# Performance work log

Measured on AMD Instinct MI355X. Metric: run time of the kernel, lower is better.

Reference implementation:

```python
import jax, jax.numpy as jnp
import numpy as np

INPUT, HIDDEN = 2048, 64

def _gru_layer(x, W_ih, W_hh, b_ih, b_hh):
    # x: [B, T, D]; returns full output sequence [B, T, H]
    B, T, _ = x.shape
    H = W_hh.shape[1]
    # precompute input projections for all timesteps: [T, B, 3H]
    xi = jnp.einsum('btd,gd->tbg', x, W_ih) + b_ih
    h0 = jnp.zeros((B, H), dtype=x.dtype)

    def step(h, xt):
        hp = h @ W_hh.T + b_hh                      # [B, 3H]
        r = jax.nn.sigmoid(xt[:, :H] + hp[:, :H])
        z = jax.nn.sigmoid(xt[:, H:2*H] + hp[:, H:2*H])
        n = jnp.tanh(xt[:, 2*H:] + r * hp[:, 2*H:])
        h_new = (1.0 - z) * n + z * h
        return h_new, h_new

    _, ys = jax.lax.scan(step, h0, xi)              # ys: [T, B, H]
    return jnp.transpose(ys, (1, 0, 2))


def setup_inputs() -> dict:
    key = jax.random.key(0)
    ks = jax.random.split(key, 12)
    B, T = 64, 512
    s0 = 1.0 / np.sqrt(HIDDEN)  # PyTorch GRU init scale
    u = lambda k, shape: jax.random.uniform(k, shape, jnp.float32, -s0, s0)
    return {
        'x': jax.random.normal(ks[0], (B, T, INPUT), jnp.float32),
        'W_ih0': u(ks[1], (3 * HIDDEN, INPUT)),
        'W_hh0': u(ks[2], (3 * HIDDEN, HIDDEN)),
        'b_ih0': u(ks[3], (3 * HIDDEN,)),
        'b_hh0': u(ks[4], (3 * HIDDEN,)),
        'W_ih1': u(ks[5], (3 * HIDDEN, HIDDEN)),
        'W_hh1': u(ks[6], (3 * HIDDEN, HIDDEN)),
        'b_ih1': u(ks[7], (3 * HIDDEN,)),
        'b_hh1': u(ks[8], (3 * HIDDEN,)),
        'fc_w': u(ks[9], (1, HIDDEN)),
        'fc_b': u(ks[10], (1,)),
    }


def reference(x, W_ih0, W_hh0, b_ih0, b_hh0, W_ih1, W_hh1, b_ih1, b_hh1, fc_w, fc_b):
    y0 = _gru_layer(x, W_ih0, W_hh0, b_ih0, b_hh0)   # [B, T, H]
    y1 = _gru_layer(y0, W_ih1, W_hh1, b_ih1, b_hh1)  # [B, T, H]
    h_last = y1[:, -1, :]                            # h_n of top layer
    return h_last @ fc_w.T + fc_b                    # [B, 1]
```

## Files before the change

kernel.cpp:

```cpp
#include <hip/hip_runtime.h>

#define T_STEPS 512
#define BATCH   64
#define HID     64
#define G3      192
#define DIN     2048
#define B_BLK   16
#define NBLK    4
#define LOG2E   1.44269504088896340736f
#define LDP     196
#define NROUND  130

typedef float    f32x4    __attribute__((ext_vector_type(4)));
typedef short    short8   __attribute__((ext_vector_type(8)));
typedef unsigned uint32x4 __attribute__((ext_vector_type(4)));

__device__ __forceinline__ unsigned short f2bf(float f) {
    unsigned int u = __builtin_bit_cast(unsigned int, f);
    unsigned int r = u + 0x7fffu + ((u >> 16) & 1u);
    return (unsigned short)(r >> 16);
}
__device__ __forceinline__ unsigned int cvtpk(float a, float b) {
    unsigned int r;
    asm("v_cvt_pk_bf16_f32 %0, %1, %2" : "=v"(r) : "v"(a), "v"(b));
    return r;
}
__device__ __forceinline__ float exp2neg(float x) {
    float r; asm("v_exp_f32 %0, -%1" : "=v"(r) : "v"(x)); return r;
}
__device__ __forceinline__ float exp2pos(float x) {
    float r; asm("v_exp_f32 %0, %1" : "=v"(r) : "v"(x)); return r;
}
__device__ __forceinline__ void wg_barrier() {
    asm volatile("s_waitcnt lgkmcnt(0)" ::: "memory");
    __builtin_amdgcn_s_barrier();
    asm volatile("" ::: "memory");
}
__device__ __forceinline__ void sig_flag(volatile unsigned* f, unsigned v) {
    asm volatile("s_waitcnt lgkmcnt(0)" ::: "memory");
    *f = v;
}
__device__ __forceinline__ void wait_flags(const unsigned* base, unsigned tag) {
    const unsigned addr = (unsigned)(unsigned long long)base;
    for (;;) {
        uint32x4 f;
        asm volatile("ds_read_b128 %0, %1\n\ts_waitcnt lgkmcnt(0)"
                     : "=v"(f) : "v"(addr) : "memory");
        unsigned m0 = f.x < f.y ? f.x : f.y;
        unsigned m1 = f.z < f.w ? f.z : f.w;
        if ((m0 < m1 ? m0 : m1) >= tag) break;
    }
    asm volatile("" ::: "memory");
}

__device__ __forceinline__ float gunit(float grs, float gzs, float a2,
                                       float xn, float h) {
    float R   = 1.f + exp2neg(grs);
    float Q   = 1.f + exp2neg(gzs);
    float r   = __builtin_amdgcn_rcpf(R);
    float s   = fmaf(r, a2, xn);
    float P   = 1.f + exp2pos(s);
    float ipq = __builtin_amdgcn_rcpf(P * Q);
    float n   = fmaf(-2.f, ipq * Q, 1.f);
    return fmaf(h - n, ipq * P, n);
}

#define BM  128
#define BK  64
#define LDA 72
#define LDB 72

__launch_bounds__(512, 1)
__global__ void proj0_kernel(const float* __restrict__ x,
                             const float* __restrict__ Wih0,
                             const float* __restrict__ bih0,
                             float* __restrict__ xi)
{
    __shared__ unsigned short Asm[BM * LDA];
    __shared__ unsigned short Bsm[G3 * LDB];

    const int tid  = threadIdx.x;
    const int wave = tid >> 6;
    const int lane = tid & 63;
    const int wm   = wave >> 2;
    const int wn   = wave & 3;
    const int m0   = blockIdx.x * BM;
    const int l16  = lane & 15;
    const int lk   = lane >> 4;
    const int rA   = tid >> 4;
    const int c4   = tid & 15;

    const float* xb = x    + (size_t)(m0 + rA) * DIN + c4 * 4;
    const float* wb = Wih0 + (size_t)rA        * DIN + c4 * 4;
    unsigned short* ap = Asm + rA * LDA + c4 * 4;
    unsigned short* bp = Bsm + rA * LDB + c4 * 4;

    f32x4 acc[4][3];
#pragma unroll
    for (int mi = 0; mi < 4; ++mi)
#pragma unroll
        for (int ni = 0; ni < 3; ++ni)
            acc[mi][ni] = (f32x4){0.f, 0.f, 0.f, 0.f};

    float4 stA[4], stB[6];
#pragma unroll
    for (int it = 0; it < 4; ++it) stA[it] = *(const float4*)(xb + it * 32 * DIN);
#pragma unroll
    for (int it = 0; it < 6; ++it) stB[it] = *(const float4*)(wb + it * 32 * DIN);

    for (int kt = 0; kt < DIN / BK; ++kt) {
#pragma unroll
        for (int it = 0; it < 4; ++it) {
            uint2 pk;
            pk.x = cvtpk(stA[it].x, stA[it].y);
            pk.y = cvtpk(stA[it].z, stA[it].w);
            *(uint2*)(ap + it * 32 * LDA) = pk;
        }
#pragma unroll
        for (int it = 0; it < 6; ++it) {
            uint2 pk;
            pk.x = cvtpk(stB[it].x, stB[it].y);
            pk.y = cvtpk(stB[it].z, stB[it].w);
            *(uint2*)(bp + it * 32 * LDB) = pk;
        }
        if (kt + 1 < DIN / BK) {
            const int kk = (kt + 1) * BK;
#pragma unroll
            for (int it = 0; it < 4; ++it) stA[it] = *(const float4*)(xb + kk + it * 32 * DIN);
#pragma unroll
            for (int it = 0; it < 6; ++it) stB[it] = *(const float4*)(wb + kk + it * 32 * DIN);
        }
        wg_barrier();

#pragma unroll
        for (int ks = 0; ks < 2; ++ks) {
            const int kb = ks * 32 + lk * 8;
            short8 a[4], bfr[3];
#pragma unroll
            for (int mi = 0; mi < 4; ++mi)
                a[mi] = *(const short8*)&Asm[(wm * 64 + mi * 16 + l16) * LDA + kb];
#pragma unroll
            for (int ni = 0; ni < 3; ++ni)
                bfr[ni] = *(const short8*)&Bsm[(wn * 48 + ni * 16 + l16) * LDB + kb];
#pragma unroll
            for (int mi = 0; mi < 4; ++mi)
#pragma unroll
                for (int ni = 0; ni < 3; ++ni)
                    acc[mi][ni] = __builtin_amdgcn_mfma_f32_16x16x32_bf16(
                        a[mi], bfr[ni], acc[mi][ni], 0, 0, 0);
        }
        wg_barrier();
    }

#pragma unroll
    for (int ni = 0; ni < 3; ++ni) {
        int g = wn * 48 + ni * 16 + l16;
        float sc = (g < 128) ? LOG2E : 2.f * LOG2E;
        float bias = bih0[g];
#pragma unroll
        for (int mi = 0; mi < 4; ++mi) {
#pragma unroll
            for (int r = 0; r < 4; ++r) {
                int m  = m0 + wm * 64 + mi * 16 + lk * 4 + r;
                int t  = m & 511;
                int bb = m >> 9;
                xi[(size_t)(t * BATCH + bb) * G3 + g] = (acc[mi][ni][r] + bias) * sc;
            }
        }
    }
}

__launch_bounds__(768, 1)
__global__ void gru_fused_kernel(const float* __restrict__ xi,
                                 const float* __restrict__ Whh0,
                                 const float* __restrict__ bhh0,
                                 const float* __restrict__ Wih1,
                                 const float* __restrict__ bih1,
                                 const float* __restrict__ Whh1,
                                 const float* __restrict__ bhh1,
                                 const float* __restrict__ fcw,
                                 const float* __restrict__ fcb,
                                 float* __restrict__ out)
{
    __shared__ __align__(16) unsigned short h0d[8][8][B_BLK][8];
    __shared__ __align__(16) unsigned short h1d[8][8][B_BLK][8];
    __shared__ __align__(16) float pbuf[8][B_BLK][LDP];
    __shared__ float fcbuf[B_BLK][68];
    __shared__ __align__(16) unsigned h0flag[4];
    __shared__ __align__(16) unsigned h1flag[4];

    const int tid  = threadIdx.x;
    const int w    = tid >> 6;
    const int l    = tid & 63;
    const int c    = l & 15;
    const int kg   = l >> 4;
    const int blk  = blockIdx.x;
    const int role = w >> 2;
    const int sub  = w & 3;
    const int jw   = sub * 16;

    short8 frag[6];
    f32x4  bC[3];
    {
        const float* Wsel = (role == 0) ? Whh0 : (role == 1) ? Wih1 : Whh1;
#pragma unroll
        for (int g = 0; g < 3; ++g) {
            const float sc = (g == 2) ? 2.f * LOG2E : LOG2E;
#pragma unroll
            for (int ks = 0; ks < 2; ++ks) {
                const size_t roff = (size_t)(g * 64 + jw + c) * HID + ks * 32 + kg * 8;
                short8 s;
#pragma unroll
                for (int j = 0; j < 8; ++j) s[j] = (short)f2bf(Wsel[roff + j] * sc);
                frag[g * 2 + ks] = s;
            }
            float4 vh0 = *(const float4*)&bhh0[g * 64 + jw + kg * 4];
            float4 vi1 = *(const float4*)&bih1[g * 64 + jw + kg * 4];
            float4 vh1 = *(const float4*)&bhh1[g * 64 + jw + kg * 4];
            if (role == 0) {
                bC[g] = (f32x4){vh0.x * sc, vh0.y * sc, vh0.z * sc, vh0.w * sc};
            } else if (role == 1) {
                if (g < 2)
                    bC[g] = (f32x4){(vi1.x + vh1.x) * sc, (vi1.y + vh1.y) * sc,
                                    (vi1.z + vh1.z) * sc, (vi1.w + vh1.w) * sc};
                else
                    bC[g] = (f32x4){vi1.x * sc, vi1.y * sc, vi1.z * sc, vi1.w * sc};
            } else {
                if (g < 2) bC[g] = (f32x4){0.f, 0.f, 0.f, 0.f};
                else       bC[g] = (f32x4){vh1.x * sc, vh1.y * sc, vh1.z * sc, vh1.w * sc};
            }
        }
    }

    float hst[4] = {0.f, 0.f, 0.f, 0.f};

    for (int i = tid; i < 4096; i += 768) {
        ((unsigned int*)h0d)[i] = 0;
        ((unsigned int*)h1d)[i] = 0;
    }
    if (tid < 4) { h0flag[tid] = 0; h1flag[tid] = 0; }
    __syncthreads();

    const int chunk = 2 * sub + (kg >> 1);
    const int coff  = (kg & 1) * 4;

    if (role == 0) {
        __builtin_amdgcn_s_setprio(2);
        const size_t xstep = (size_t)BATCH * G3;
        const float* xp = xi + (size_t)(blk * B_BLK + c) * G3 + jw + kg * 4;
        float4 pA[3], pB[3];
        pA[0] = *(const float4*)(xp);
        pA[1] = *(const float4*)(xp + 64);
        pA[2] = *(const float4*)(xp + 128);
        pB[0] = *(const float4*)(xp + xstep);
        pB[1] = *(const float4*)(xp + xstep + 64);
        pB[2] = *(const float4*)(xp + xstep + 128);
        const float* xpr = xp + 2 * xstep;

        auto stepL0 = [&](int t, int s, float4 (&cur)[3]) {
            if (s > 0) {
                __builtin_amdgcn_s_setprio(0);
                wait_flags(h0flag, (unsigned)t);
                __builtin_amdgcn_s_setprio(2);
            }
            const int pb = (t + 7) & 7;
            short8 x0 = *(const short8*)&h0d[pb][kg][c][0];
            short8 x1 = *(const short8*)&h0d[pb][4 + kg][c][0];
            f32x4 a0 = bC[0], a1 = bC[1], a2 = bC[2];
            a0 = __builtin_amdgcn_mfma_f32_16x16x32_bf16(frag[0], x0, a0, 0, 0, 0);
            a0 = __builtin_amdgcn_mfma_f32_16x16x32_bf16(frag[1], x1, a0, 0, 0, 0);
            a1 = __builtin_amdgcn_mfma_f32_16x16x32_bf16(frag[2], x0, a1, 0, 0, 0);
            a1 = __builtin_amdgcn_mfma_f32_16x16x32_bf16(frag[3], x1, a1, 0, 0, 0);
            a2 = __builtin_amdgcn_mfma_f32_16x16x32_bf16(frag[4], x0, a2, 0, 0, 0);
            a2 = __builtin_amdgcn_mfma_f32_16x16x32_bf16(frag[5], x1, a2, 0, 0, 0);

            float4 xr4 = cur[0], xz4 = cur[1], xn4 = cur[2];
            if (t + 2 < T_STEPS) {
                cur[0] = *(const float4*)(xpr);
                cur[1] = *(const float4*)(xpr + 64);
                cur[2] = *(const float4*)(xpr + 128);
                xpr += xstep;
            }
            hst[0] = gunit(xr4.x + a0[0], xz4.x + a1[0], a2[0], xn4.x, hst[0]);
            hst[1] = gunit(xr4.y + a0[1], xz4.y + a1[1], a2[1], xn4.y, hst[1]);
            hst[2] = gunit(xr4.z + a0[2], xz4.z + a1[2], a2[2], xn4.z, hst[2]);
            hst[3] = gunit(xr4.w + a0[3], xz4.w + a1[3], a2[3], xn4.w, hst[3]);
            uint2 hw;
            hw.x = cvtpk(hst[0], hst[1]);
            hw.y = cvtpk(hst[2], hst[3]);
            *(uint2*)&h0d[t & 7][chunk][c][coff] = hw;
            if (s < 3) sig_flag(&h0flag[sub], (unsigned)(t + 1));
        };

        for (int r = 0; r < NROUND; ++r) {
            if (r < 128) {
                const int t0 = 4 * r;
                stepL0(t0 + 0, 0, pA);
                stepL0(t0 + 1, 1, pB);
                stepL0(t0 + 2, 2, pA);
                stepL0(t0 + 3, 3, pB);
            }
            wg_barrier();
        }
    } else if (role == 1) {
        auto stepP = [&](int k) {
            const int pb = k & 7;
            short8 x0 = *(const short8*)&h0d[pb][kg][c][0];
            short8 x1 = *(const short8*)&h0d[pb][4 + kg][c][0];
            f32x4 p0 = bC[0], p1 = bC[1], p2 = bC[2];
            p0 = __builtin_amdgcn_mfma_f32_16x16x32_bf16(frag[0], x0, p0, 0, 0, 0);
            p0 = __builtin_amdgcn_mfma_f32_16x16x32_bf16(frag[1], x1, p0, 0, 0, 0);
            p1 = __builtin_amdgcn_mfma_f32_16x16x32_bf16(frag[2], x0, p1, 0, 0, 0);
            p1 = __builtin_amdgcn_mfma_f32_16x16x32_bf16(frag[3], x1, p1, 0, 0, 0);
            p2 = __builtin_amdgcn_mfma_f32_16x16x32_bf16(frag[4], x0, p2, 0, 0, 0);
            p2 = __builtin_amdgcn_mfma_f32_16x16x32_bf16(frag[5], x1, p2, 0, 0, 0);
            float* pd = &pbuf[k & 7][c][jw + kg * 4];
            *(f32x4*)(pd)       = p0;
            *(f32x4*)(pd + 64)  = p1;
            *(f32x4*)(pd + 128) = p2;
        };
        for (int r = 0; r < NROUND; ++r) {
            if (r >= 1 && r <= 128) {
                const int k0 = 4 * r - 4;
                stepP(k0 + 0);
                stepP(k0 + 1);
                stepP(k0 + 2);
                stepP(k0 + 3);
            }
            wg_barrier();
        }
    } else {
        auto stepL1 = [&](int k, int s) {
            if (s > 0) wait_flags(h1flag, (unsigned)k);
            const int py = (k + 7) & 7;
            short8 y0 = *(const short8*)&h1d[py][kg][c][0];
            short8 y1 = *(const short8*)&h1d[py][4 + kg][c][0];
            f32x4 g0 = bC[0], g1 = bC[1], g2 = bC[2];
            g0 = __builtin_amdgcn_mfma_f32_16x16x32_bf16(frag[0], y0, g0, 0, 0, 0);
            g0 = __builtin_amdgcn_mfma_f32_16x16x32_bf16(frag[1], y1, g0, 0, 0, 0);
            g1 = __builtin_amdgcn_mfma_f32_16x16x32_bf16(frag[2], y0, g1, 0, 0, 0);
            g1 = __builtin_amdgcn_mfma_f32_16x16x32_bf16(frag[3], y1, g1, 0, 0, 0);
            g2 = __builtin_amdgcn_mfma_f32_16x16x32_bf16(frag[4], y0, g2, 0, 0, 0);
            g2 = __builtin_amdgcn_mfma_f32_16x16x32_bf16(frag[5], y1, g2, 0, 0, 0);

            const float* pd = &pbuf[k & 7][c][jw + kg * 4];
            f32x4 pr = *(const f32x4*)(pd);
            f32x4 pz = *(const f32x4*)(pd + 64);
            f32x4 pn = *(const f32x4*)(pd + 128);
#pragma unroll
            for (int q = 0; q < 4; ++q)
                hst[q] = gunit(pr[q] + g0[q], pz[q] + g1[q], g2[q], pn[q], hst[q]);
            uint2 hw;
            hw.x = cvtpk(hst[0], hst[1]);
            hw.y = cvtpk(hst[2], hst[3]);
            *(uint2*)&h1d[k & 7][chunk][c][coff] = hw;
            if (s < 3) sig_flag(&h1flag[sub], (unsigned)(k + 1));
        };
        for (int r = 0; r < NROUND; ++r) {
            if (r >= 2) {
                const int k0 = 4 * r - 8;
                stepL1(k0 + 0, 0);
                stepL1(k0 + 1, 1);
                stepL1(k0 + 2, 2);
                stepL1(k0 + 3, 3);
            }
            wg_barrier();
        }
    }

    if (role == 2) {
#pragma unroll
        for (int q = 0; q < 4; ++q)
            fcbuf[c][jw + kg * 4 + q] = hst[q];
    }
    __syncthreads();
    if (w == 0) {
        float p = 0.f;
#pragma unroll
        for (int jj = 0; jj < 16; ++jj)
            p += fcbuf[c][kg * 16 + jj] * fcw[kg * 16 + jj];
        p += __shfl_xor(p, 16);
        p += __shfl_xor(p, 32);
        if (kg == 0) out[blk * B_BLK + c] = p + fcb[0];
    }
}

extern "C" void kernel_launch(void* const* d_in, const int* in_sizes, int n_in,
                              void* d_out, int out_size, void* d_ws, size_t ws_size,
                              hipStream_t stream)
{
    const float* x    = (const float*)d_in[0];
    const float* Wih0 = (const float*)d_in[1];
    const float* Whh0 = (const float*)d_in[2];
    const float* bih0 = (const float*)d_in[3];
    const float* bhh0 = (const float*)d_in[4];
    const float* Wih1 = (const float*)d_in[5];
    const float* Whh1 = (const float*)d_in[6];
    const float* bih1 = (const float*)d_in[7];
    const float* bhh1 = (const float*)d_in[8];
    const float* fcw  = (const float*)d_in[9];
    const float* fcb  = (const float*)d_in[10];
    float* out = (float*)d_out;
    float* xi  = (float*)d_ws;

    hipLaunchKernelGGL(proj0_kernel, dim3(32768 / BM), dim3(512), 0, stream,
                       x, Wih0, bih0, xi);
    hipLaunchKernelGGL(gru_fused_kernel, dim3(NBLK), dim3(768), 0, stream,
                       xi, Whh0, bhh0, Wih1, bih1, Whh1, bhh1, fcw, fcb, out);
}
```

Measured before the change: 344.8 us.

## Fuse input projection into recurrent kernel with per-chunk ready flags

Merges the layer-0 input projection GEMM and the recurrent GRU kernel into one launch. Blocks 0-3 run the recurrence and blocks 4+ compute projection tiles ordered by time chunk, publishing completion through global atomic counters. The recurrence spins on those counters so it can start before the whole projection finishes. The projection output is also stored as bf16 to halve its traffic. This adds spin-wait and forward-progress risk (it relies on the recurrent blocks being co-resident with the producer blocks) and lowers the precision of the intermediate.

```diff
diff --git a/kernel.cpp b/kernel.cpp
--- a/kernel.cpp
+++ b/kernel.cpp
@@ -6,10 +6,13 @@
 #define G3      192
 #define DIN     2048
 #define B_BLK   16
-#define NBLK    4
 #define LOG2E   1.44269504088896340736f
 #define LDP     196
 #define NROUND  130
+#define LDA     72
+#define LDB     72
+#define PBM     64
+#define PBK     64
 
 typedef float    f32x4    __attribute__((ext_vector_type(4)));
 typedef short    short8   __attribute__((ext_vector_type(8)));
@@ -24,6 +27,12 @@
     unsigned int r;
     asm("v_cvt_pk_bf16_f32 %0, %1, %2" : "=v"(r) : "v"(a), "v"(b));
     return r;
+}
+__device__ __forceinline__ float bflo(unsigned int u) {
+    return __builtin_bit_cast(float, u << 16);
+}
+__device__ __forceinline__ float bfhi(unsigned int u) {
+    return __builtin_bit_cast(float, u & 0xffff0000u);
 }
 __device__ __forceinline__ float exp2neg(float x) {
     float r; asm("v_exp_f32 %0, -%1" : "=v"(r) : "v"(x)); return r;
@@ -51,6 +60,10 @@
         if ((m0 < m1 ? m0 : m1) >= tag) break;
     }
     asm volatile("" ::: "memory");
+}
+__device__ __forceinline__ void wait_chunk(const unsigned* cp) {
+    while (__hip_atomic_load(cp, __ATOMIC_ACQUIRE, __HIP_MEMORY_SCOPE_AGENT) < 16u)
+        __builtin_amdgcn_s_sleep(8);
 }
 
 __device__ __forceinline__ float gunit(float grs, float gzs, float a2,
@@ -65,131 +78,135 @@
     return fmaf(h - n, ipq * P, n);
 }
 
-#define BM  128
-#define BK  64
-#define LDA 72
-#define LDB 72
-
-__launch_bounds__(512, 1)
-__global__ void proj0_kernel(const float* __restrict__ x,
+struct GruS {
+    unsigned h0flag[4];
+    unsigned h1flag[4];
+    unsigned short h0d[8][8][B_BLK][8];
+    unsigned short h1d[8][8][B_BLK][8];
+    float pbuf[8][B_BLK][LDP];
+    float fcbuf[B_BLK][68];
+};
+struct ProjS {
+    unsigned short Asm[PBM * LDA];
+    unsigned short Bsm[G3 * LDB];
+};
+#define SMEM_BYTES 137504
+
+__global__ void zero_flags_kernel(unsigned* cnt) {
+    if (threadIdx.x < 64) cnt[threadIdx.x] = 0;
+}
+
+__launch_bounds__(768, 1)
+__global__ void fused_kernel(const float* __restrict__ x,
                              const float* __restrict__ Wih0,
                              const float* __restrict__ bih0,
-                             float* __restrict__ xi)
+                             const float* __restrict__ Whh0,
+                             const float* __restrict__ bhh0,
+                             const float* __restrict__ Wih1,
+                             const float* __restrict__ bih1,
+                             const float* __restrict__ Whh1,
+                             const float* __restrict__ bhh1,
+                             const float* __restrict__ fcw,
+                             const float* __restrict__ fcb,
+                             unsigned short* __restrict__ xi,
+                             unsigned* __restrict__ cnt,
+                             float* __restrict__ out)
 {
-    __shared__ unsigned short Asm[BM * LDA];
-    __shared__ unsigned short Bsm[G3 * LDB];
-
-    const int tid  = threadIdx.x;
-    const int wave = tid >> 6;
-    const int lane = tid & 63;
-    const int wm   = wave >> 2;
-    const int wn   = wave & 3;
-    const int m0   = blockIdx.x * BM;
-    const int l16  = lane & 15;
-    const int lk   = lane >> 4;
-    const int rA   = tid >> 4;
-    const int c4   = tid & 15;
-
-    const float* xb = x    + (size_t)(m0 + rA) * DIN + c4 * 4;
-    const float* wb = Wih0 + (size_t)rA        * DIN + c4 * 4;
-    unsigned short* ap = Asm + rA * LDA + c4 * 4;
-    unsigned short* bp = Bsm + rA * LDB + c4 * 4;
-
-    f32x4 acc[4][3];
-#pragma unroll
-    for (int mi = 0; mi < 4; ++mi)
-#pragma unroll
-        for (int ni = 0; ni < 3; ++ni)
-            acc[mi][ni] = (f32x4){0.f, 0.f, 0.f, 0.f};
-
-    float4 stA[4], stB[6];
-#pragma unroll
-    for (int it = 0; it < 4; ++it) stA[it] = *(const float4*)(xb + it * 32 * DIN);
-#pragma unroll
-    for (int it = 0; it < 6; ++it) stB[it] = *(const float4*)(wb + it * 32 * DIN);
-
-    for (int kt = 0; kt < DIN / BK; ++kt) {
-#pragma unroll
-        for (int it = 0; it < 4; ++it) {
-            uint2 pk;
-            pk.x = cvtpk(stA[it].x, stA[it].y);
-            pk.y = cvtpk(stA[it].z, stA[it].w);
-            *(uint2*)(ap + it * 32 * LDA) = pk;
-        }
-#pragma unroll
-        for (int it = 0; it < 6; ++it) {
-            uint2 pk;
-            pk.x = cvtpk(stB[it].x, stB[it].y);
-            pk.y = cvtpk(stB[it].z, stB[it].w);
-            *(uint2*)(bp + it * 32 * LDB) = pk;
-        }
-        if (kt + 1 < DIN / BK) {
-            const int kk = (kt + 1) * BK;
-#pragma unroll
-            for (int it = 0; it < 4; ++it) stA[it] = *(const float4*)(xb + kk + it * 32 * DIN);
-#pragma unroll
-            for (int it = 0; it < 6; ++it) stB[it] = *(const float4*)(wb + kk + it * 32 * DIN);
-        }
-        wg_barrier();
-
-#pragma unroll
-        for (int ks = 0; ks < 2; ++ks) {
-            const int kb = ks * 32 + lk * 8;
-            short8 a[4], bfr[3];
-#pragma unroll
-            for (int mi = 0; mi < 4; ++mi)
-                a[mi] = *(const short8*)&Asm[(wm * 64 + mi * 16 + l16) * LDA + kb];
-#pragma unroll
-            for (int ni = 0; ni < 3; ++ni)
-                bfr[ni] = *(const short8*)&Bsm[(wn * 48 + ni * 16 + l16) * LDB + kb];
-#pragma unroll
-            for (int mi = 0; mi < 4; ++mi)
-#pragma unroll
-                for (int ni = 0; ni < 3; ++ni)
-                    acc[mi][ni] = __builtin_amdgcn_mfma_f32_16x16x32_bf16(
-                        a[mi], bfr[ni], acc[mi][ni], 0, 0, 0);
-        }
-        wg_barrier();
-    }
-
-#pragma unroll
-    for (int ni = 0; ni < 3; ++ni) {
-        int g = wn * 48 + ni * 16 + l16;
-        float sc = (g < 128) ? LOG2E : 2.f * LOG2E;
-        float bias = bih0[g];
-#pragma unroll
-        for (int mi = 0; mi < 4; ++mi) {
-#pragma unroll
-            for (int r = 0; r < 4; ++r) {
-                int m  = m0 + wm * 64 + mi * 16 + lk * 4 + r;
-                int t  = m & 511;
-                int bb = m >> 9;
-                xi[(size_t)(t * BATCH + bb) * G3 + g] = (acc[mi][ni][r] + bias) * sc;
-            }
-        }
-    }
-}
-
-__launch_bounds__(768, 1)
-__global__ void gru_fused_kernel(const float* __restrict__ xi,
-                                 const float* __restrict__ Whh0,
-                                 const float* __restrict__ bhh0,
-                                 const float* __restrict__ Wih1,
-                                 const float* __restrict__ bih1,
-                                 const float* __restrict__ Whh1,
-                                 const float* __restrict__ bhh1,
-                                 const float* __restrict__ fcw,
-                                 const float* __restrict__ fcb,
-                                 float* __restrict__ out)
-{
-    __shared__ __align__(16) unsigned short h0d[8][8][B_BLK][8];
-    __shared__ __align__(16) unsigned short h1d[8][8][B_BLK][8];
-    __shared__ __align__(16) float pbuf[8][B_BLK][LDP];
-    __shared__ float fcbuf[B_BLK][68];
-    __shared__ __align__(16) unsigned h0flag[4];
-    __shared__ __align__(16) unsigned h1flag[4];
-
-    const int tid  = threadIdx.x;
+    __shared__ __align__(16) unsigned char smem[SMEM_BYTES];
+    const int tid = threadIdx.x;
+
+    if (blockIdx.x >= 4) {
+        auto& PJ = *reinterpret_cast<ProjS*>(smem);
+        const int p   = blockIdx.x - 4;
+        const int b   = p & 63;
+        const int ch  = p >> 6;
+        const int m0  = b * 512 + ch * 64;
+        const int w   = tid >> 6;
+        const int lane = tid & 63;
+        const int wm  = w & 1;
+        const int wn  = w >> 1;
+        const int l16 = lane & 15;
+        const int lk  = lane >> 4;
+
+        f32x4 acc[2][2];
+#pragma unroll
+        for (int mi = 0; mi < 2; ++mi)
+#pragma unroll
+            for (int ni = 0; ni < 2; ++ni)
+                acc[mi][ni] = (f32x4){0.f, 0.f, 0.f, 0.f};
+
+        float4 a0, a1, b0, b1, b2, b3;
+        auto loadT = [&](int kk) {
+            { int u = tid;       a0 = *(const float4*)&x[(size_t)(m0 + (u >> 4)) * DIN + kk + (u & 15) * 4]; }
+            if (tid < 256) { int u = tid + 768; a1 = *(const float4*)&x[(size_t)(m0 + (u >> 4)) * DIN + kk + (u & 15) * 4]; }
+            { int u = tid;        b0 = *(const float4*)&Wih0[(size_t)(u >> 4) * DIN + kk + (u & 15) * 4]; }
+            { int u = tid + 768;  b1 = *(const float4*)&Wih0[(size_t)(u >> 4) * DIN + kk + (u & 15) * 4]; }
+            { int u = tid + 1536; b2 = *(const float4*)&Wih0[(size_t)(u >> 4) * DIN + kk + (u & 15) * 4]; }
+            { int u = tid + 2304; b3 = *(const float4*)&Wih0[(size_t)(u >> 4) * DIN + kk + (u & 15) * 4]; }
+        };
+        auto packT = [&]() {
+            { int u = tid;       uint2 pk = {cvtpk(a0.x, a0.y), cvtpk(a0.z, a0.w)};
+              *(uint2*)&PJ.Asm[(u >> 4) * LDA + (u & 15) * 4] = pk; }
+            if (tid < 256) { int u = tid + 768; uint2 pk = {cvtpk(a1.x, a1.y), cvtpk(a1.z, a1.w)};
+              *(uint2*)&PJ.Asm[(u >> 4) * LDA + (u & 15) * 4] = pk; }
+            { int u = tid;        uint2 pk = {cvtpk(b0.x, b0.y), cvtpk(b0.z, b0.w)};
+              *(uint2*)&PJ.Bsm[(u >> 4) * LDB + (u & 15) * 4] = pk; }
+            { int u = tid + 768;  uint2 pk = {cvtpk(b1.x, b1.y), cvtpk(b1.z, b1.w)};
+              *(uint2*)&PJ.Bsm[(u >> 4) * LDB + (u & 15) * 4] = pk; }
+            { int u = tid + 1536; uint2 pk = {cvtpk(b2.x, b2.y), cvtpk(b2.z, b2.w)};
+              *(uint2*)&PJ.Bsm[(u >> 4) * LDB + (u & 15) * 4] = pk; }
+            { int u = tid + 2304; uint2 pk = {cvtpk(b3.x, b3.y), cvtpk(b3.z, b3.w)};
+              *(uint2*)&PJ.Bsm[(u >> 4) * LDB + (u & 15) * 4] = pk; }
+        };
+
+        loadT(0);
+        for (int kt = 0; kt < DIN / PBK; ++kt) {
+            packT();
+            if (kt + 1 < DIN / PBK) loadT((kt + 1) * PBK);
+            wg_barrier();
+#pragma unroll
+            for (int ks = 0; ks < 2; ++ks) {
+                const int kb = ks * 32 + lk * 8;
+                short8 af[2], bf[2];
+#pragma unroll
+                for (int mi = 0; mi < 2; ++mi)
+                    af[mi] = *(const short8*)&PJ.Asm[(wm * 32 + mi * 16 + l16) * LDA + kb];
+#pragma unroll
+                for (int ni = 0; ni < 2; ++ni)
+                    bf[ni] = *(const short8*)&PJ.Bsm[(wn * 32 + ni * 16 + l16) * LDB + kb];
+#pragma unroll
+                for (int mi = 0; mi < 2; ++mi)
+#pragma unroll
+                    for (int ni = 0; ni < 2; ++ni)
+                        acc[mi][ni] = __builtin_amdgcn_mfma_f32_16x16x32_bf16(
+                            af[mi], bf[ni], acc[mi][ni], 0, 0, 0);
+            }
+            wg_barrier();
+        }
+
+#pragma unroll
+        for (int ni = 0; ni < 2; ++ni) {
+            int g = wn * 32 + ni * 16 + l16;
+            float sc = (g < 128) ? LOG2E : 2.f * LOG2E;
+            float bias = bih0[g];
+#pragma unroll
+            for (int mi = 0; mi < 2; ++mi) {
+#pragma unroll
+                for (int r = 0; r < 4; ++r) {
+                    int m = m0 + wm * 32 + mi * 16 + lk * 4 + r;
+                    int t = m & 511;
+                    xi[(size_t)(t * BATCH + b) * G3 + g] = f2bf((acc[mi][ni][r] + bias) * sc);
+                }
+            }
+        }
+        __threadfence();
+        __syncthreads();
+        if (tid == 0)
+            atomicAdd(&cnt[(b >> 4) * 8 + ch], 1u);
+        return;
+    }
+
+    auto& S = *reinterpret_cast<GruS*>(smem);
     const int w    = tid >> 6;
     const int l    = tid & 63;
     const int c    = l & 15;
@@ -234,38 +251,40 @@
 
     float hst[4] = {0.f, 0.f, 0.f, 0.f};
 
-    for (int i = tid; i < 4096; i += 768) {
-        ((unsigned int*)h0d)[i] = 0;
-        ((unsigned int*)h1d)[i] = 0;
-    }
-    if (tid < 4) { h0flag[tid] = 0; h1flag[tid] = 0; }
+    {
+        unsigned* hz = (unsigned*)&S.h0d[0][0][0][0];
+        for (int i = tid; i < 8192; i += 768) hz[i] = 0;
+    }
+    if (tid < 4) { S.h0flag[tid] = 0; S.h1flag[tid] = 0; }
     __syncthreads();
 
     const int chunk = 2 * sub + (kg >> 1);
     const int coff  = (kg & 1) * 4;
 
     if (role == 0) {
+        const size_t xstep = (size_t)BATCH * G3;
+        const unsigned short* xp =
+            xi + (size_t)(blk * B_BLK + c) * G3 + jw + kg * 4;
+        wait_chunk(&cnt[blk * 8 + 0]);
         __builtin_amdgcn_s_setprio(2);
-        const size_t xstep = (size_t)BATCH * G3;
-        const float* xp = xi + (size_t)(blk * B_BLK + c) * G3 + jw + kg * 4;
-        float4 pA[3], pB[3];
-        pA[0] = *(const float4*)(xp);
-        pA[1] = *(const float4*)(xp + 64);
-        pA[2] = *(const float4*)(xp + 128);
-        pB[0] = *(const float4*)(xp + xstep);
-        pB[1] = *(const float4*)(xp + xstep + 64);
-        pB[2] = *(const float4*)(xp + xstep + 128);
-        const float* xpr = xp + 2 * xstep;
-
-        auto stepL0 = [&](int t, int s, float4 (&cur)[3]) {
+        uint2 pA[3], pB[3];
+        pA[0] = *(const uint2*)(xp);
+        pA[1] = *(const uint2*)(xp + 64);
+        pA[2] = *(const uint2*)(xp + 128);
+        pB[0] = *(const uint2*)(xp + xstep);
+        pB[1] = *(const uint2*)(xp + xstep + 64);
+        pB[2] = *(const uint2*)(xp + xstep + 128);
+        const unsigned short* xpr = xp + 2 * xstep;
+
+        auto stepL0 = [&](int t, int s, uint2 (&cur)[3]) {
             if (s > 0) {
                 __builtin_amdgcn_s_setprio(0);
-                wait_flags(h0flag, (unsigned)t);
+                wait_flags(S.h0flag, (unsigned)t);
                 __builtin_amdgcn_s_setprio(2);
             }
             const int pb = (t + 7) & 7;
-            short8 x0 = *(const short8*)&h0d[pb][kg][c][0];
-            short8 x1 = *(const short8*)&h0d[pb][4 + kg][c][0];
+            short8 x0 = *(const short8*)&S.h0d[pb][kg][c][0];
+            short8 x1 = *(const short8*)&S.h0d[pb][4 + kg][c][0];
             f32x4 a0 = bC[0], a1 = bC[1], a2 = bC[2];
             a0 = __builtin_amdgcn_mfma_f32_16x16x32_bf16(frag[0], x0, a0, 0, 0, 0);
             a0 = __builtin_amdgcn_mfma_f32_16x16x32_bf16(frag[1], x1, a0, 0, 0, 0);
@@ -274,22 +293,30 @@
             a2 = __builtin_amdgcn_mfma_f32_16x16x32_bf16(frag[4], x0, a2, 0, 0, 0);
             a2 = __builtin_amdgcn_mfma_f32_16x16x32_bf16(frag[5], x1, a2, 0, 0, 0);
 
-            float4 xr4 = cur[0], xz4 = cur[1], xn4 = cur[2];
-            if (t + 2 < T_STEPS) {
-                cur[0] = *(const float4*)(xpr);
-                cur[1] = *(const float4*)(xpr + 64);
-                cur[2] = *(const float4*)(xpr + 128);
+            float xrf[4] = {bflo(cur[0].x), bfhi(cur[0].x), bflo(cur[0].y), bfhi(cur[0].y)};
+            float xzf[4] = {bflo(cur[1].x), bfhi(cur[1].x), bflo(cur[1].y), bfhi(cur[1].y)};
+            float xnf[4] = {bflo(cur[2].x), bfhi(cur[2].x), bflo(cur[2].y), bfhi(cur[2].y)};
+            const int tn = t + 2;
+            if (tn < T_STEPS) {
+                if ((tn & 63) == 0) {
+                    __builtin_amdgcn_s_setprio(0);
+                    wait_chunk(&cnt[blk * 8 + (tn >> 6)]);
+                    __builtin_amdgcn_s_setprio(2);
+                }
+                cur[0] = *(const uint2*)(xpr);
+                cur[1] = *(const uint2*)(xpr + 64);
+                cur[2] = *(const uint2*)(xpr + 128);
                 xpr += xstep;
             }
-            hst[0] = gunit(xr4.x + a0[0], xz4.x + a1[0], a2[0], xn4.x, hst[0]);
-            hst[1] = gunit(xr4.y + a0[1], xz4.y + a1[1], a2[1], xn4.y, hst[1]);
-            hst[2] = gunit(xr4.z + a0[2], xz4.z + a1[2], a2[2], xn4.z, hst[2]);
-            hst[3] = gunit(xr4.w + a0[3], xz4.w + a1[3], a2[3], xn4.w, hst[3]);
+            hst[0] = gunit(xrf[0] + a0[0], xzf[0] + a1[0], a2[0], xnf[0], hst[0]);
+            hst[1] = gunit(xrf[1] + a0[1], xzf[1] + a1[1], a2[1], xnf[1], hst[1]);
+            hst[2] = gunit(xrf[2] + a0[2], xzf[2] + a1[2], a2[2], xnf[2], hst[2]);
+            hst[3] = gunit(xrf[3] + a0[3], xzf[3] + a1[3], a2[3], xnf[3], hst[3]);
             uint2 hw;
             hw.x = cvtpk(hst[0], hst[1]);
             hw.y = cvtpk(hst[2], hst[3]);
-            *(uint2*)&h0d[t & 7][chunk][c][coff] = hw;
-            if (s < 3) sig_flag(&h0flag[sub], (unsigned)(t + 1));
+            *(uint2*)&S.h0d[t & 7][chunk][c][coff] = hw;
+            if (s < 3) sig_flag(&S.h0flag[sub], (unsigned)(t + 1));
         };
 
         for (int r = 0; r < NROUND; ++r) {
@@ -305,8 +332,8 @@
     } else if (role == 1) {
         auto stepP = [&](int k) {
             const int pb = k & 7;
-            short8 x0 = *(const short8*)&h0d[pb][kg][c][0];
-            short8 x1 = *(const short8*)&h0d[pb][4 + kg][c][0];
+            short8 x0 = *(const short8*)&S.h0d[pb][kg][c][0];
+            short8 x1 = *(const short8*)&S.h0d[pb][4 + kg][c][0];
             f32x4 p0 = bC[0], p1 = bC[1], p2 = bC[2];
             p0 = __builtin_amdgcn_mfma_f32_16x16x32_bf16(frag[0], x0, p0, 0, 0, 0);
             p0 = __builtin_amdgcn_mfma_f32_16x16x32_bf16(frag[1], x1, p0, 0, 0, 0);
@@ -314,7 +341,7 @@
             p1 = __builtin_amdgcn_mfma_f32_16x16x32_bf16(frag[3], x1, p1, 0, 0, 0);
             p2 = __builtin_amdgcn_mfma_f32_16x16x32_bf16(frag[4], x0, p2, 0, 0, 0);
             p2 = __builtin_amdgcn_mfma_f32_16x16x32_bf16(frag[5], x1, p2, 0, 0, 0);
-            float* pd = &pbuf[k & 7][c][jw + kg * 4];
+            float* pd = &S.pbuf[k & 7][c][jw + kg * 4];
             *(f32x4*)(pd)       = p0;
             *(f32x4*)(pd + 64)  = p1;
             *(f32x4*)(pd + 128) = p2;
@@ -331,10 +358,10 @@
         }
     } else {
         auto stepL1 = [&](int k, int s) {
-            if (s > 0) wait_flags(h1flag, (unsigned)k);
+            if (s > 0) wait_flags(S.h1flag, (unsigned)k);
             const int py = (k + 7) & 7;
-            short8 y0 = *(const short8*)&h1d[py][kg][c][0];
-            short8 y1 = *(const short8*)&h1d[py][4 + kg][c][0];
+            short8 y0 = *(const short8*)&S.h1d[py][kg][c][0];
+            short8 y1 = *(const short8*)&S.h1d[py][4 + kg][c][0];
             f32x4 g0 = bC[0], g1 = bC[1], g2 = bC[2];
             g0 = __builtin_amdgcn_mfma_f32_16x16x32_bf16(frag[0], y0, g0, 0, 0, 0);
             g0 = __builtin_amdgcn_mfma_f32_16x16x32_bf16(frag[1], y1, g0, 0, 0, 0);
@@ -343,7 +370,7 @@
             g2 = __builtin_amdgcn_mfma_f32_16x16x32_bf16(frag[4], y0, g2, 0, 0, 0);
             g2 = __builtin_amdgcn_mfma_f32_16x16x32_bf16(frag[5], y1, g2, 0, 0, 0);
 
-            const float* pd = &pbuf[k & 7][c][jw + kg * 4];
+            const float* pd = &S.pbuf[k & 7][c][jw + kg * 4];
             f32x4 pr = *(const f32x4*)(pd);
             f32x4 pz = *(const f32x4*)(pd + 64);
             f32x4 pn = *(const f32x4*)(pd + 128);
@@ -353,8 +380,8 @@
             uint2 hw;
             hw.x = cvtpk(hst[0], hst[1]);
             hw.y = cvtpk(hst[2], hst[3]);
-            *(uint2*)&h1d[k & 7][chunk][c][coff] = hw;
-            if (s < 3) sig_flag(&h1flag[sub], (unsigned)(k + 1));
+            *(uint2*)&S.h1d[k & 7][chunk][c][coff] = hw;
+            if (s < 3) sig_flag(&S.h1flag[sub], (unsigned)(k + 1));
         };
         for (int r = 0; r < NROUND; ++r) {
             if (r >= 2) {
@@ -371,17 +398,17 @@
     if (role == 2) {
 #pragma unroll
         for (int q = 0; q < 4; ++q)
-            fcbuf[c][jw + kg * 4 + q] = hst[q];
+            S.fcbuf[c][jw + kg * 4 + q] = hst[q];
     }
     __syncthreads();
     if (w == 0) {
-        float p = 0.f;
+        float pv = 0.f;
 #pragma unroll
         for (int jj = 0; jj < 16; ++jj)
-            p += fcbuf[c][kg * 16 + jj] * fcw[kg * 16 + jj];
-        p += __shfl_xor(p, 16);
-        p += __shfl_xor(p, 32);
-        if (kg == 0) out[blk * B_BLK + c] = p + fcb[0];
+            pv += S.fcbuf[c][kg * 16 + jj] * fcw[kg * 16 + jj];
+        pv += __shfl_xor(pv, 16);
+        pv += __shfl_xor(pv, 32);
+        if (kg == 0) out[blk * B_BLK + c] = pv + fcb[0];
     }
 }
 
@@ -401,10 +428,12 @@
     const float* fcw  = (const float*)d_in[9];
     const float* fcb  = (const float*)d_in[10];
     float* out = (float*)d_out;
-    float* xi  = (float*)d_ws;
-
-    hipLaunchKernelGGL(proj0_kernel, dim3(32768 / BM), dim3(512), 0, stream,
-                       x, Wih0, bih0, xi);
-    hipLaunchKernelGGL(gru_fused_kernel, dim3(NBLK), dim3(768), 0, stream,
-                       xi, Whh0, bhh0, Wih1, bih1, Whh1, bhh1, fcw, fcb, out);
-}
+
+    unsigned* cnt       = (unsigned*)d_ws;
+    unsigned short* xi  = (unsigned short*)((char*)d_ws + 4096);
+
+    hipLaunchKernelGGL(zero_flags_kernel, dim3(1), dim3(64), 0, stream, cnt);
+    hipLaunchKernelGGL(fused_kernel, dim3(516), dim3(768), 0, stream,
+                       x, Wih0, bih0, Whh0, bhh0, Wih1, bih1, Whh1, bhh1,
+                       fcw, fcb, xi, cnt, out);
+}
```

New measurement: 530.4 us. 1.54x slower.
